# Optimization experiments

Measured on AMD Instinct MI355X. Metric: run time of the kernel, lower is better.

Reference implementation:

```python
import jax, jax.numpy as jnp
import numpy as np

MUL = 128
LS = [0, 1, 2]
D1 = [MUL * (2 * l + 1) for l in LS]            # per-irrep dims of x1 / out: 128, 384, 640
D2 = [2 * l + 1 for l in LS]                    # per-irrep dims of x2 (mul=1): 1, 3, 5
O1 = np.concatenate([[0], np.cumsum(D1)])       # offsets into x1 / out
O2 = np.concatenate([[0], np.cumsum(D2)])       # offsets into x2
PATHS = [(l1, l2, lo) for l1 in LS for l2 in LS for lo in LS
         if abs(l1 - l2) <= lo <= l1 + l2]      # 15 sorted 'uvw' instructions
DIM_OUT = int(sum(D1))

def _count():
    # fan-in count per output position: each 'uvw' path adds mul_1*mul_2 = 128
    c = np.zeros(DIM_OUT, dtype=np.float32)
    for (_, _, lo) in PATHS:
        c[O1[lo]:O1[lo] + D1[lo]] += MUL * 1
    return np.maximum(c, 1.0)

COUNT = jnp.asarray(_count())

def setup_inputs() -> dict:
    key = jax.random.key(0)
    ks = jax.random.split(key, 3 + len(PATHS))
    N = 16384
    inp = {
        "x1": jax.random.normal(ks[0], (N, int(sum(D1))), jnp.float32),
        "x2": jax.random.normal(ks[1], (N, int(sum(D2))), jnp.float32),
        "ws": jax.random.normal(ks[2], (len(PATHS), MUL, 1, MUL), jnp.float32),
    }
    for p, (l1, l2, lo) in enumerate(PATHS):
        inp[f"c{p}"] = jax.random.normal(ks[3 + p], (2 * l1 + 1, 2 * l2 + 1, 2 * lo + 1), jnp.float32)
    return inp

def _forward(x1, x2, ws, cs):
    N = x1.shape[0]
    out = jnp.zeros((N, DIM_OUT), x1.dtype)
    for p, (l1, l2, lo) in enumerate(PATHS):
        # s1: [N, mul1, 2l1+1]; s2: [N, mul2=1, 2l2+1]
        s1 = x1[:, int(O1[l1]):int(O1[l1] + D1[l1])].reshape(N, MUL, 2 * l1 + 1)
        s2 = x2[:, int(O2[l2]):int(O2[l2] + D2[l2])].reshape(N, 1, 2 * l2 + 1)
        # weighted CG contraction: ws[p] [u,v,w], cs[p] [i,j,k]
        contrib = jnp.einsum('uvw,ijk,zui,zvj->zwk', ws[p], cs[p], s1, s2)
        out = out.at[:, int(O1[lo]):int(O1[lo] + D1[lo])].add(contrib.reshape(N, D1[lo]))
    # fan-in (component) normalization
    return out / jnp.sqrt(COUNT)

def reference(x1, x2, ws, c0, c1, c2, c3, c4, c5, c6, c7, c8, c9, c10, c11, c12, c13, c14):
    cs = [c0, c1, c2, c3, c4, c5, c6, c7, c8, c9, c10, c11, c12, c13, c14]
    return _forward(x1, x2, ws, cs)
```

## Files before the change

kernel.cpp:

```cpp
#include <hip/hip_runtime.h>
#include <hip/hip_bf16.h>

typedef float f32x4 __attribute__((ext_vector_type(4)));
typedef short bf16x8 __attribute__((ext_vector_type(8)));

#define ZT 16
#define TL_STRIDE 136
#define TL_BUF (80 * TL_STRIDE)
#define YL_BUF 448

constexpr int cL1[15]  = {0,0,0,1,1,1,1,1,1,2,2,2,2,2,2};
constexpr int cL2[15]  = {0,1,2,0,1,1,1,2,2,0,1,1,2,2,2};
constexpr int cLO[15]  = {0,1,2,1,0,1,2,1,2,2,1,2,0,1,2};
constexpr int cCSZ[15] = {1,9,25,9,9,27,45,45,75,25,45,75,25,75,125};
constexpr int cCOFF[15]= {0,1,10,35,44,53,80,125,170,245,270,315,390,415,490};
constexpr int cO1[3] = {0,128,512};
constexpr int cO2[3] = {0,1,4};
constexpr int cX1O[3]= {0,1,4};

struct CP { const float* p[15]; };

__device__ __forceinline__ ushort f2bf(float f) {
    union { __hip_bfloat16 h; ushort u; } c;
    c.h = __float2bfloat16(f);
    return c.u;
}

__global__ void prep_w(const float* __restrict__ ws, ushort* __restrict__ wb) {
    __shared__ float lds[64 * 132];
    const int p = blockIdx.x;
    const int tid = threadIdx.x;
    const float* src = ws + (size_t)p * 16384;
    ushort* dst = wb + (size_t)p * 16384;
    for (int half = 0; half < 2; ++half) {
        for (int i = tid; i < 8192; i += 256) {
            int u = i >> 7, w = i & 127;
            lds[u * 132 + w] = src[(half * 64 + u) * 128 + w];
        }
        __syncthreads();
        for (int i = tid; i < 8192; i += 256) {
            int w = i >> 6, u = i & 63;
            dst[w * 128 + half * 64 + u] = f2bf(lds[u * 132 + w]);
        }
        __syncthreads();
    }
}

template<int P>
__device__ __forceinline__ void compute_y(int tid, const float* __restrict__ cl,
                                          const float* __restrict__ x2l,
                                          float* __restrict__ ybuf) {
    constexpr int l2 = cL2[P], lo = cLO[P];
    constexpr int d1 = 2*cL1[P]+1, d2 = 2*l2+1, dO = 2*lo+1;
    constexpr int span = d1 * dO;
    constexpr int span_pad = (span + 3) & ~3;
    constexpr int ny = ZT * span_pad;
    for (int idx = tid; idx < ny; idx += 256) {
        const int z = idx / span_pad, rem = idx - z * span_pad;
        float s = 0.f;
        if (rem < span) {
            const int i = rem / dO, k = rem - i * dO;
            #pragma unroll
            for (int j = 0; j < d2; ++j)
                s += cl[cCOFF[P] + (i*d2 + j)*dO + k] * x2l[z*9 + cO2[l2] + j];
        }
        ybuf[idx] = s;
    }
}

template<int P>
__device__ __forceinline__ void path_iter(
    int tid, const ushort* __restrict__ Wb, const float* __restrict__ Wsrc, int use_prep,
    const float (&x1r)[4][2][9],
    float* __restrict__ yl, ushort* __restrict__ Tl,
    const float* __restrict__ cl, const float* __restrict__ x2l,
    f32x4 (&A0)[2][1], f32x4 (&A1)[2][3], f32x4 (&A2)[2][5])
{
    constexpr int l1 = cL1[P], lo = cLO[P];
    constexpr int d1 = 2*l1+1, dO = 2*lo+1;
    constexpr int span = d1 * dO;
    constexpr int span_pad = (span + 3) & ~3;
    const int lane = tid & 63, wv = tid >> 6;

    ushort* Tcur = Tl + (P & 1) * TL_BUF;
    const float* ycur = yl + (P & 1) * YL_BUF;

    bf16x8 aP[2][4];
    if (use_prep) {
        const ushort* wp = Wb + P * 16384;
        #pragma unroll
        for (int mt = 0; mt < 2; ++mt)
        #pragma unroll
        for (int ks = 0; ks < 4; ++ks) {
            const int wrow = wv*32 + mt*16 + (lane & 15);
            const int k0   = ks*32 + ((lane >> 4) << 3);
            aP[mt][ks] = *reinterpret_cast<const bf16x8*>(wp + wrow*128 + k0);
        }
    } else {
        const float* wp = Wsrc + P * 16384;
        #pragma unroll
        for (int mt = 0; mt < 2; ++mt)
        #pragma unroll
        for (int ks = 0; ks < 4; ++ks) {
            const int wrow = wv*32 + mt*16 + (lane & 15);
            const int k0   = ks*32 + ((lane >> 4) << 3);
            bf16x8 v;
            #pragma unroll
            for (int e = 0; e < 8; ++e) v[e] = (short)f2bf(wp[(k0 + e)*128 + wrow]);
            aP[mt][ks] = v;
        }
    }

    {
        const int u0 = 2 * lane;
        #pragma unroll
        for (int r = 0; r < 4; ++r) {
            const int z = wv * 4 + r;
            f32x4 yv[span_pad / 4];
            #pragma unroll
            for (int j = 0; j < span_pad / 4; ++j)
                yv[j] = *reinterpret_cast<const f32x4*>(ycur + z * span_pad + 4 * j);
            #pragma unroll
            for (int k = 0; k < dO; ++k) {
                float s0 = 0.f, s1 = 0.f;
                #pragma unroll
                for (int i = 0; i < d1; ++i) {
                    constexpr int base = 0;  (void)base;
                    const int yi = i * dO + k;
                    const float yf = yv[yi >> 2][yi & 3];
                    s0 += x1r[r][0][cX1O[l1] + i] * yf;
                    s1 += x1r[r][1][cX1O[l1] + i] * yf;
                }
                union { uint u32; ushort h[2]; } pk;
                pk.h[0] = f2bf(s0);
                pk.h[1] = f2bf(s1);
                *reinterpret_cast<uint*>(Tcur + (z * dO + k) * TL_STRIDE + u0) = pk.u32;
            }
        }
    }

    if constexpr (P < 14)
        compute_y<P + 1>(tid, cl, x2l, yl + ((P + 1) & 1) * YL_BUF);

    __syncthreads();

    #pragma unroll
    for (int ks = 0; ks < 4; ++ks) {
        const int k0 = ks*32 + ((lane >> 4) << 3);
        #pragma unroll
        for (int nt = 0; nt < dO; ++nt) {
            const bf16x8 b = *reinterpret_cast<const bf16x8*>(
                Tcur + (nt*16 + (lane & 15))*TL_STRIDE + k0);
            if constexpr (lo == 0) {
                A0[0][nt] = __builtin_amdgcn_mfma_f32_16x16x32_bf16(aP[0][ks], b, A0[0][nt], 0,0,0);
                A0[1][nt] = __builtin_amdgcn_mfma_f32_16x16x32_bf16(aP[1][ks], b, A0[1][nt], 0,0,0);
            } else if constexpr (lo == 1) {
                A1[0][nt] = __builtin_amdgcn_mfma_f32_16x16x32_bf16(aP[0][ks], b, A1[0][nt], 0,0,0);
                A1[1][nt] = __builtin_amdgcn_mfma_f32_16x16x32_bf16(aP[1][ks], b, A1[1][nt], 0,0,0);
            } else {
                A2[0][nt] = __builtin_amdgcn_mfma_f32_16x16x32_bf16(aP[0][ks], b, A2[0][nt], 0,0,0);
                A2[1][nt] = __builtin_amdgcn_mfma_f32_16x16x32_bf16(aP[1][ks], b, A2[1][nt], 0,0,0);
            }
        }
    }
}

template<int LO, int NT>
__device__ __forceinline__ void stage_lo(const f32x4 (&A)[2][NT], float* __restrict__ stage,
                                         int c, int wv, int rg, int cw, float scale)
{
    constexpr int dO = 2*LO + 1;
    #pragma unroll
    for (int nt = 0; nt < NT; ++nt) {
        const int col = nt*16 + cw;
        const int z = col / dO, k = col - z*dO;
        if ((z >> 2) == c) {
            #pragma unroll
            for (int mt = 0; mt < 2; ++mt) {
                const int row = wv*32 + mt*16 + rg;
                float* p = stage + (z & 3)*1152 + cO1[LO] + row*dO + k;
                #pragma unroll
                for (int r = 0; r < 4; ++r) p[r*dO] = A[mt][nt][r] * scale;
            }
        }
    }
}

__global__ __launch_bounds__(256, 2)
void tp_main(const float* __restrict__ x1, const float* __restrict__ x2,
             const float* __restrict__ wsrc, const ushort* __restrict__ wb,
             int use_prep, CP cp, float* __restrict__ out)
{
    __shared__ __align__(16) ushort Tl[2 * TL_BUF];
    __shared__ __align__(16) float yl[2 * YL_BUF];
    __shared__ float cl[615];
    __shared__ float x2l[ZT * 9];

    const int tid = threadIdx.x;
    const int z0 = blockIdx.x * ZT;
    const int lane = tid & 63, wv = tid >> 6;

    #pragma unroll
    for (int p = 0; p < 15; ++p)
        for (int i = tid; i < cCSZ[p]; i += 256) cl[cCOFF[p] + i] = cp.p[p][i];
    for (int i = tid; i < ZT * 9; i += 256) x2l[i] = x2[(size_t)z0 * 9 + i];

    float x1r[4][2][9];
    #pragma unroll
    for (int r = 0; r < 4; ++r) {
        const float* b = x1 + (size_t)(z0 + wv*4 + r) * 1152;
        {
            const float2 t = *reinterpret_cast<const float2*>(b + 2*lane);
            x1r[r][0][0] = t.x; x1r[r][1][0] = t.y;
        }
        {
            float f6[6];
            #pragma unroll
            for (int j = 0; j < 3; ++j) {
                const float2 t = *reinterpret_cast<const float2*>(b + 128 + 6*lane + 2*j);
                f6[2*j] = t.x; f6[2*j + 1] = t.y;
            }
            #pragma unroll
            for (int i = 0; i < 3; ++i) { x1r[r][0][1+i] = f6[i]; x1r[r][1][1+i] = f6[3+i]; }
        }
        {
            float f10[10];
            #pragma unroll
            for (int j = 0; j < 5; ++j) {
                const float2 t = *reinterpret_cast<const float2*>(b + 512 + 10*lane + 2*j);
                f10[2*j] = t.x; f10[2*j + 1] = t.y;
            }
            #pragma unroll
            for (int i = 0; i < 5; ++i) { x1r[r][0][4+i] = f10[i]; x1r[r][1][4+i] = f10[5+i]; }
        }
    }

    f32x4 A0[2][1], A1[2][3], A2[2][5];
    #pragma unroll
    for (int mt = 0; mt < 2; ++mt) {
        A0[mt][0] = (f32x4){0.f, 0.f, 0.f, 0.f};
        #pragma unroll
        for (int nt = 0; nt < 3; ++nt) A1[mt][nt] = (f32x4){0.f, 0.f, 0.f, 0.f};
        #pragma unroll
        for (int nt = 0; nt < 5; ++nt) A2[mt][nt] = (f32x4){0.f, 0.f, 0.f, 0.f};
    }

    __syncthreads();
    compute_y<0>(tid, cl, x2l, yl);
    __syncthreads();

    path_iter< 0>(tid, wb, wsrc, use_prep, x1r, yl, Tl, cl, x2l, A0, A1, A2);
    path_iter< 1>(tid, wb, wsrc, use_prep, x1r, yl, Tl, cl, x2l, A0, A1, A2);
    path_iter< 2>(tid, wb, wsrc, use_prep, x1r, yl, Tl, cl, x2l, A0, A1, A2);
    path_iter< 3>(tid, wb, wsrc, use_prep, x1r, yl, Tl, cl, x2l, A0, A1, A2);
    path_iter< 4>(tid, wb, wsrc, use_prep, x1r, yl, Tl, cl, x2l, A0, A1, A2);
    path_iter< 5>(tid, wb, wsrc, use_prep, x1r, yl, Tl, cl, x2l, A0, A1, A2);
    path_iter< 6>(tid, wb, wsrc, use_prep, x1r, yl, Tl, cl, x2l, A0, A1, A2);
    path_iter< 7>(tid, wb, wsrc, use_prep, x1r, yl, Tl, cl, x2l, A0, A1, A2);
    path_iter< 8>(tid, wb, wsrc, use_prep, x1r, yl, Tl, cl, x2l, A0, A1, A2);
    path_iter< 9>(tid, wb, wsrc, use_prep, x1r, yl, Tl, cl, x2l, A0, A1, A2);
    path_iter<10>(tid, wb, wsrc, use_prep, x1r, yl, Tl, cl, x2l, A0, A1, A2);
    path_iter<11>(tid, wb, wsrc, use_prep, x1r, yl, Tl, cl, x2l, A0, A1, A2);
    path_iter<12>(tid, wb, wsrc, use_prep, x1r, yl, Tl, cl, x2l, A0, A1, A2);
    path_iter<13>(tid, wb, wsrc, use_prep, x1r, yl, Tl, cl, x2l, A0, A1, A2);
    path_iter<14>(tid, wb, wsrc, use_prep, x1r, yl, Tl, cl, x2l, A0, A1, A2);

    const int rg = (lane >> 4) << 2, cw = lane & 15;
    float* stage = (float*)Tl;
    #pragma unroll
    for (int c = 0; c < 4; ++c) {
        __syncthreads();
        stage_lo<0, 1>(A0, stage, c, wv, rg, cw, 0.05103103630798288f);
        stage_lo<1, 3>(A1, stage, c, wv, rg, cw, 0.03608439182435161f);
        stage_lo<2, 5>(A2, stage, c, wv, rg, cw, 0.03608439182435161f);
        __syncthreads();
        float4* dst = (float4*)(out + (size_t)(z0 + 4*c) * 1152);
        const float4* src = (const float4*)stage;
        #pragma unroll
        for (int it = 0; it < 5; ++it) {
            const int idx = it * 256 + tid;
            if (idx < 1152) dst[idx] = src[idx];
        }
    }
}

extern "C" void kernel_launch(void* const* d_in, const int* in_sizes, int n_in,
                              void* d_out, int out_size, void* d_ws, size_t ws_size,
                              hipStream_t stream) {
    const float* x1 = (const float*)d_in[0];
    const float* x2 = (const float*)d_in[1];
    const float* ws = (const float*)d_in[2];
    CP cp;
    for (int p = 0; p < 15; ++p) cp.p[p] = (const float*)d_in[3 + p];
    float* out = (float*)d_out;

    const int N = in_sizes[0] / 1152;
    const int use_prep = (ws_size >= (size_t)(15 * 128 * 128 * 2)) ? 1 : 0;

    if (use_prep)
        prep_w<<<15, 256, 0, stream>>>(ws, (ushort*)d_ws);
    tp_main<<<N / ZT, 256, 0, stream>>>(x1, x2, ws, (const ushort*)d_ws,
                                        use_prep, cp, out);
}
```

Measured before the change: 93.52 us.

## Reorder paths into compact LDS ring with XOR swizzle and raise occupancy

Replaces the padded double-buffered T tile (stride 136) with a 16K-element ring. Paths run in a new order, with per-step offsets chosen so consecutive paths' tiles do not overlap, and an XOR swizzle replaces the padding to avoid LDS bank conflicts. The MFMA operand roles are swapped (T as A, weights as B) and the accumulator layout and epilogue staging are adjusted to match. Launch bounds go from 2 to 4 blocks per CU, relying on the smaller LDS footprint, at the risk of register pressure or spills and tricky ring-overlap correctness.

```diff
diff --git a/kernel.cpp b/kernel.cpp
--- a/kernel.cpp
+++ b/kernel.cpp
@@ -5,8 +5,7 @@
 typedef short bf16x8 __attribute__((ext_vector_type(8)));
 
 #define ZT 16
-#define TL_STRIDE 136
-#define TL_BUF (80 * TL_STRIDE)
+#define TL_RING 16384
 #define YL_BUF 448
 
 constexpr int cL1[15]  = {0,0,0,1,1,1,1,1,1,2,2,2,2,2,2};
@@ -17,6 +16,9 @@
 constexpr int cO1[3] = {0,128,512};
 constexpr int cO2[3] = {0,1,4};
 constexpr int cX1O[3]= {0,1,4};
+
+constexpr int cSEQ [15] = {2,0,6,4,8,12,9,1,11,3,14,5,13,7,10};
+constexpr int cROFF[15] = {0,80,0,80,0,80,0,80,0,80,0,80,0,48,0};
 
 struct CP { const float* p[15]; };
 
@@ -68,46 +70,47 @@
     }
 }
 
-template<int P>
+template<int S>
 __device__ __forceinline__ void path_iter(
     int tid, const ushort* __restrict__ Wb, const float* __restrict__ Wsrc, int use_prep,
     const float (&x1r)[4][2][9],
     float* __restrict__ yl, ushort* __restrict__ Tl,
     const float* __restrict__ cl, const float* __restrict__ x2l,
-    f32x4 (&A0)[2][1], f32x4 (&A1)[2][3], f32x4 (&A2)[2][5])
+    f32x4 (&A0)[1][2], f32x4 (&A1)[3][2], f32x4 (&A2)[5][2])
 {
+    constexpr int P = cSEQ[S];
     constexpr int l1 = cL1[P], lo = cLO[P];
     constexpr int d1 = 2*l1+1, dO = 2*lo+1;
     constexpr int span = d1 * dO;
     constexpr int span_pad = (span + 3) & ~3;
     const int lane = tid & 63, wv = tid >> 6;
 
-    ushort* Tcur = Tl + (P & 1) * TL_BUF;
-    const float* ycur = yl + (P & 1) * YL_BUF;
+    ushort* Tcur = Tl + cROFF[S] * 128;
+    const float* ycur = yl + (S & 1) * YL_BUF;
 
     bf16x8 aP[2][4];
     if (use_prep) {
         const ushort* wp = Wb + P * 16384;
         #pragma unroll
-        for (int mt = 0; mt < 2; ++mt)
+        for (int nt = 0; nt < 2; ++nt)
         #pragma unroll
         for (int ks = 0; ks < 4; ++ks) {
-            const int wrow = wv*32 + mt*16 + (lane & 15);
+            const int wrow = wv*32 + nt*16 + (lane & 15);
             const int k0   = ks*32 + ((lane >> 4) << 3);
-            aP[mt][ks] = *reinterpret_cast<const bf16x8*>(wp + wrow*128 + k0);
+            aP[nt][ks] = *reinterpret_cast<const bf16x8*>(wp + wrow*128 + k0);
         }
     } else {
         const float* wp = Wsrc + P * 16384;
         #pragma unroll
-        for (int mt = 0; mt < 2; ++mt)
+        for (int nt = 0; nt < 2; ++nt)
         #pragma unroll
         for (int ks = 0; ks < 4; ++ks) {
-            const int wrow = wv*32 + mt*16 + (lane & 15);
+            const int wrow = wv*32 + nt*16 + (lane & 15);
             const int k0   = ks*32 + ((lane >> 4) << 3);
             bf16x8 v;
             #pragma unroll
             for (int e = 0; e < 8; ++e) v[e] = (short)f2bf(wp[(k0 + e)*128 + wrow]);
-            aP[mt][ks] = v;
+            aP[nt][ks] = v;
         }
     }
 
@@ -122,10 +125,10 @@
                 yv[j] = *reinterpret_cast<const f32x4*>(ycur + z * span_pad + 4 * j);
             #pragma unroll
             for (int k = 0; k < dO; ++k) {
+                const int col = z * dO + k;
                 float s0 = 0.f, s1 = 0.f;
                 #pragma unroll
                 for (int i = 0; i < d1; ++i) {
-                    constexpr int base = 0;  (void)base;
                     const int yi = i * dO + k;
                     const float yf = yv[yi >> 2][yi & 3];
                     s0 += x1r[r][0][cX1O[l1] + i] * yf;
@@ -134,64 +137,66 @@
                 union { uint u32; ushort h[2]; } pk;
                 pk.h[0] = f2bf(s0);
                 pk.h[1] = f2bf(s1);
-                *reinterpret_cast<uint*>(Tcur + (z * dO + k) * TL_STRIDE + u0) = pk.u32;
-            }
-        }
-    }
-
-    if constexpr (P < 14)
-        compute_y<P + 1>(tid, cl, x2l, yl + ((P + 1) & 1) * YL_BUF);
+                const uint idx = (uint)(col * 128 + u0) ^ (uint)((col & 7) << 3);
+                *reinterpret_cast<uint*>(Tcur + idx) = pk.u32;
+            }
+        }
+    }
+
+    if constexpr (S < 14)
+        compute_y<cSEQ[S + 1]>(tid, cl, x2l, yl + ((S + 1) & 1) * YL_BUF);
 
     __syncthreads();
 
     #pragma unroll
-    for (int ks = 0; ks < 4; ++ks) {
-        const int k0 = ks*32 + ((lane >> 4) << 3);
-        #pragma unroll
-        for (int nt = 0; nt < dO; ++nt) {
-            const bf16x8 b = *reinterpret_cast<const bf16x8*>(
-                Tcur + (nt*16 + (lane & 15))*TL_STRIDE + k0);
+    for (int t = 0; t < dO; ++t) {
+        #pragma unroll
+        for (int ks = 0; ks < 4; ++ks) {
+            const int col = t*16 + (lane & 15);
+            const int k0  = ks*32 + ((lane >> 4) << 3);
+            const uint idx = (uint)(col * 128 + k0) ^ (uint)((col & 7) << 3);
+            const bf16x8 a = *reinterpret_cast<const bf16x8*>(Tcur + idx);
             if constexpr (lo == 0) {
-                A0[0][nt] = __builtin_amdgcn_mfma_f32_16x16x32_bf16(aP[0][ks], b, A0[0][nt], 0,0,0);
-                A0[1][nt] = __builtin_amdgcn_mfma_f32_16x16x32_bf16(aP[1][ks], b, A0[1][nt], 0,0,0);
+                A0[t][0] = __builtin_amdgcn_mfma_f32_16x16x32_bf16(a, aP[0][ks], A0[t][0], 0,0,0);
+                A0[t][1] = __builtin_amdgcn_mfma_f32_16x16x32_bf16(a, aP[1][ks], A0[t][1], 0,0,0);
             } else if constexpr (lo == 1) {
-                A1[0][nt] = __builtin_amdgcn_mfma_f32_16x16x32_bf16(aP[0][ks], b, A1[0][nt], 0,0,0);
-                A1[1][nt] = __builtin_amdgcn_mfma_f32_16x16x32_bf16(aP[1][ks], b, A1[1][nt], 0,0,0);
+                A1[t][0] = __builtin_amdgcn_mfma_f32_16x16x32_bf16(a, aP[0][ks], A1[t][0], 0,0,0);
+                A1[t][1] = __builtin_amdgcn_mfma_f32_16x16x32_bf16(a, aP[1][ks], A1[t][1], 0,0,0);
             } else {
-                A2[0][nt] = __builtin_amdgcn_mfma_f32_16x16x32_bf16(aP[0][ks], b, A2[0][nt], 0,0,0);
-                A2[1][nt] = __builtin_amdgcn_mfma_f32_16x16x32_bf16(aP[1][ks], b, A2[1][nt], 0,0,0);
-            }
-        }
-    }
-}
-
-template<int LO, int NT>
-__device__ __forceinline__ void stage_lo(const f32x4 (&A)[2][NT], float* __restrict__ stage,
-                                         int c, int wv, int rg, int cw, float scale)
+                A2[t][0] = __builtin_amdgcn_mfma_f32_16x16x32_bf16(a, aP[0][ks], A2[t][0], 0,0,0);
+                A2[t][1] = __builtin_amdgcn_mfma_f32_16x16x32_bf16(a, aP[1][ks], A2[t][1], 0,0,0);
+            }
+        }
+    }
+}
+
+template<int LO, int NTILES>
+__device__ __forceinline__ void stage_lo(const f32x4 (&A)[NTILES][2], float* __restrict__ stage,
+                                         int c, int wv, int g, int m, float scale)
 {
     constexpr int dO = 2*LO + 1;
     #pragma unroll
-    for (int nt = 0; nt < NT; ++nt) {
-        const int col = nt*16 + cw;
-        const int z = col / dO, k = col - z*dO;
+    for (int t = 0; t < NTILES; ++t)
+    #pragma unroll
+    for (int r = 0; r < 4; ++r) {
+        const int zcol = t*16 + g*4 + r;
+        const int z = zcol / dO, k = zcol - z*dO;
         if ((z >> 2) == c) {
             #pragma unroll
-            for (int mt = 0; mt < 2; ++mt) {
-                const int row = wv*32 + mt*16 + rg;
-                float* p = stage + (z & 3)*1152 + cO1[LO] + row*dO + k;
-                #pragma unroll
-                for (int r = 0; r < 4; ++r) p[r*dO] = A[mt][nt][r] * scale;
-            }
-        }
-    }
-}
-
-__global__ __launch_bounds__(256, 2)
+            for (int nt = 0; nt < 2; ++nt) {
+                const int w = wv*32 + nt*16 + m;
+                stage[(z & 3)*1152 + cO1[LO] + w*dO + k] = A[t][nt][r] * scale;
+            }
+        }
+    }
+}
+
+__global__ __launch_bounds__(256, 4)
 void tp_main(const float* __restrict__ x1, const float* __restrict__ x2,
              const float* __restrict__ wsrc, const ushort* __restrict__ wb,
              int use_prep, CP cp, float* __restrict__ out)
 {
-    __shared__ __align__(16) ushort Tl[2 * TL_BUF];
+    __shared__ __align__(16) ushort Tl[TL_RING];
     __shared__ __align__(16) float yl[2 * YL_BUF];
     __shared__ float cl[615];
     __shared__ float x2l[ZT * 9];
@@ -235,18 +240,18 @@
         }
     }
 
-    f32x4 A0[2][1], A1[2][3], A2[2][5];
-    #pragma unroll
-    for (int mt = 0; mt < 2; ++mt) {
-        A0[mt][0] = (f32x4){0.f, 0.f, 0.f, 0.f};
-        #pragma unroll
-        for (int nt = 0; nt < 3; ++nt) A1[mt][nt] = (f32x4){0.f, 0.f, 0.f, 0.f};
-        #pragma unroll
-        for (int nt = 0; nt < 5; ++nt) A2[mt][nt] = (f32x4){0.f, 0.f, 0.f, 0.f};
+    f32x4 A0[1][2], A1[3][2], A2[5][2];
+    #pragma unroll
+    for (int nt = 0; nt < 2; ++nt) {
+        A0[0][nt] = (f32x4){0.f, 0.f, 0.f, 0.f};
+        #pragma unroll
+        for (int t = 0; t < 3; ++t) A1[t][nt] = (f32x4){0.f, 0.f, 0.f, 0.f};
+        #pragma unroll
+        for (int t = 0; t < 5; ++t) A2[t][nt] = (f32x4){0.f, 0.f, 0.f, 0.f};
     }
 
     __syncthreads();
-    compute_y<0>(tid, cl, x2l, yl);
+    compute_y<cSEQ[0]>(tid, cl, x2l, yl);
     __syncthreads();
 
     path_iter< 0>(tid, wb, wsrc, use_prep, x1r, yl, Tl, cl, x2l, A0, A1, A2);
@@ -265,14 +270,14 @@
     path_iter<13>(tid, wb, wsrc, use_prep, x1r, yl, Tl, cl, x2l, A0, A1, A2);
     path_iter<14>(tid, wb, wsrc, use_prep, x1r, yl, Tl, cl, x2l, A0, A1, A2);
 
-    const int rg = (lane >> 4) << 2, cw = lane & 15;
+    const int g = lane >> 4, m = lane & 15;
     float* stage = (float*)Tl;
     #pragma unroll
     for (int c = 0; c < 4; ++c) {
         __syncthreads();
-        stage_lo<0, 1>(A0, stage, c, wv, rg, cw, 0.05103103630798288f);
-        stage_lo<1, 3>(A1, stage, c, wv, rg, cw, 0.03608439182435161f);
-        stage_lo<2, 5>(A2, stage, c, wv, rg, cw, 0.03608439182435161f);
+        stage_lo<0, 1>(A0, stage, c, wv, g, m, 0.05103103630798288f);
+        stage_lo<1, 3>(A1, stage, c, wv, g, m, 0.03608439182435161f);
+        stage_lo<2, 5>(A2, stage, c, wv, g, m, 0.03608439182435161f);
         __syncthreads();
         float4* dst = (float4*)(out + (size_t)(z0 + 4*c) * 1152);
         const float4* src = (const float4*)stage;
```

After: 327.9 us. 251% more time.
